# Optimization experiments

Hardware: AMD Instinct MI355X
Metric: run time of the kernel (lower is better)

Reference implementation:

```python
import jax, jax.numpy as jnp
import numpy as np

N_WIRES = 6
DIM = 1 << N_WIRES  # 64, equals input channel dim C for amplitude encoding
HID = N_WIRES       # hidden_dim = len(ops)


def _rx(theta):
    c = jnp.cos(theta / 2).astype(jnp.complex64)
    s = jnp.sin(theta / 2).astype(jnp.complex64)
    return jnp.stack([jnp.stack([c, -1j * s]), jnp.stack([-1j * s, c])])


def _ry(theta):
    c = jnp.cos(theta / 2).astype(jnp.complex64)
    s = jnp.sin(theta / 2).astype(jnp.complex64)
    return jnp.stack([jnp.stack([c, -s]), jnp.stack([s, c])])


def _apply_1q(state, U, wire):
    # state: (N, 2, 2, ..., 2); apply 2x2 U on qubit axis wire+1
    s = jnp.moveaxis(state, wire + 1, 1)
    s = jnp.einsum('ab,nb...->na...', U, s)
    return jnp.moveaxis(s, 1, wire + 1)


def _apply_cnot(state, c, t):
    # flip target axis where control bit == 1
    s = jnp.moveaxis(state, (c + 1, t + 1), (1, 2))
    s = jnp.concatenate([s[:, :1], jnp.flip(s[:, 1:2], axis=2)], axis=1)
    return jnp.moveaxis(s, (1, 2), (c + 1, t + 1))


def _expval_z(state, wire):
    # <Z_wire> = P(bit=0) - P(bit=1)
    p = state.real ** 2 + state.imag ** 2
    p = jnp.moveaxis(p, wire + 1, 1).reshape(p.shape[0], 2, -1)
    return p[:, 0].sum(-1) - p[:, 1].sum(-1)


def _value_layer(x_flat, params, qk):
    # amplitude encoding: normalize input into state amplitudes (C == DIM)
    norm = jnp.linalg.norm(x_flat, axis=-1, keepdims=True)
    psi = (x_flat / norm).astype(jnp.complex64)
    state = psi.reshape((x_flat.shape[0],) + (2,) * N_WIRES)
    rx0, ry0, ry1 = params[0], params[1], params[2]
    for j in range(N_WIRES):
        state = _apply_1q(state, _rx(rx0[j]), j)
        state = _apply_1q(state, _ry(ry0[j]), j)
    for j in range(N_WIRES):
        state = _apply_cnot(state, j, (j + 1) % N_WIRES)
    for j in range(N_WIRES):
        state = _apply_1q(state, _ry(ry1[j]), j)
    if qk:
        z0 = _expval_z(state, 0)
        return jnp.stack([z0] * HID, axis=-1)  # qk=True replicates wire-0 <Z>
    return jnp.stack([_expval_z(state, w) for w in range(N_WIRES)], axis=-1)


def setup_inputs() -> dict:
    key = jax.random.key(0)
    k1, k2, k3, k4 = jax.random.split(key, 4)
    B, T, C = 16, 2048, DIM
    return {
        'x': jax.random.normal(k1, (B, T, C), dtype=jnp.float32),
        'params_q': jax.random.normal(k2, (3, N_WIRES), dtype=jnp.float32),
        'params_k': jax.random.normal(k3, (3, N_WIRES), dtype=jnp.float32),
        'params_v': jax.random.normal(k4, (3, N_WIRES), dtype=jnp.float32),
    }


def reference(x, params_q, params_k, params_v):
    B, T, C = x.shape
    xf = x.reshape(B * T, C)
    q = _value_layer(xf, params_q, True).reshape(B, T, HID)
    k = _value_layer(xf, params_k, True).reshape(B, T, HID)
    v = _value_layer(xf, params_v, False).reshape(B, T, HID)
    scores = jnp.einsum('btd,bsd->bts', q, k) / jnp.sqrt(jnp.float32(HID))
    attn = jax.nn.softmax(scores, axis=-1)
    return jnp.einsum('bts,bsd->btd', attn, v)
```

## Files before the change

kernel.cpp:

```cpp
#include <hip/hip_runtime.h>
#include <math.h>

#define NWIRES 6
#define DIM 64
#define NTOK 32768
#define NBATCH 16
#define TPB 2048
#define NMOM 16
#define SQRT6F 2.4494897427831781f

__global__ void qsa_prep(const float* __restrict__ pq,
                         const float* __restrict__ pk,
                         const float* __restrict__ pv,
                         float* __restrict__ cs) {
    int i = threadIdx.x;
    if (i >= 54) return;
    int circ = i / 18, g = i % 18;
    const float* p = (circ == 0) ? pq : (circ == 1 ? pk : pv);
    float s, c;
    sincosf(0.5f * p[g], &s, &c);
    cs[i * 2 + 0] = c;
    cs[i * 2 + 1] = s;
}

__device__ __forceinline__ float pswap(float v) { return __shfl_xor(v, 1, 64); }

template<int M>
__device__ __forceinline__ void rx_l(float* re, float* im, float c, float s) {
#pragma unroll
    for (int i = 0; i < 32; ++i) {
        if (i & M) continue;
        int j = i | M;
        float r0 = re[i], i0 = im[i], r1 = re[j], i1 = im[j];
        re[i] = c * r0 + s * i1;
        im[i] = c * i0 - s * r1;
        re[j] = c * r1 + s * i0;
        im[j] = c * i1 - s * r0;
    }
}

template<int M>
__device__ __forceinline__ void ry_l(float* re, float* im, float c, float s) {
#pragma unroll
    for (int i = 0; i < 32; ++i) {
        if (i & M) continue;
        int j = i | M;
        float r0 = re[i], i0 = im[i], r1 = re[j], i1 = im[j];
        re[i] = c * r0 - s * r1;
        im[i] = c * i0 - s * i1;
        re[j] = c * r1 + s * r0;
        im[j] = c * i1 + s * i0;
    }
}

template<int MC, int MT>
__device__ __forceinline__ void cnot_l(float* re, float* im) {
#pragma unroll
    for (int i = 0; i < 32; ++i) {
        if (!(i & MC) || (i & MT)) continue;
        int j = i | MT;
        float tr = re[i]; re[i] = re[j]; re[j] = tr;
        float ti = im[i]; im[i] = im[j]; im[j] = ti;
    }
}

__device__ __forceinline__ void rx_s(float* re, float* im, float c, float s) {
#pragma unroll
    for (int i = 0; i < 32; ++i) {
        float pre = pswap(re[i]), pim = pswap(im[i]);
        re[i] = c * re[i] + s * pim;
        im[i] = c * im[i] - s * pre;
    }
}

__device__ __forceinline__ void ry_s(float* re, float* im, float c, float ss) {
#pragma unroll
    for (int i = 0; i < 32; ++i) {
        float pre = pswap(re[i]), pim = pswap(im[i]);
        re[i] = c * re[i] + ss * pre;
        im[i] = c * im[i] + ss * pim;
    }
}

__device__ __forceinline__ void cnot_c01(float* re, float* im, int p) {
#pragma unroll
    for (int i = 0; i < 32; ++i) {
        if (i & 16) continue;
        int j = i | 16;
        float r0 = re[i], r1 = re[j], i0 = im[i], i1 = im[j];
        re[i] = p ? r1 : r0;  re[j] = p ? r0 : r1;
        im[i] = p ? i1 : i0;  im[j] = p ? i0 : i1;
    }
}

__device__ __forceinline__ void cnot_c50(float* re, float* im) {
#pragma unroll
    for (int i = 1; i < 32; i += 2) {
        re[i] = pswap(re[i]);
        im[i] = pswap(im[i]);
    }
}

__global__ __attribute__((amdgpu_waves_per_eu(4, 8)))
__launch_bounds__(64) void qsa_sim(
        const float* __restrict__ x,
        const float* __restrict__ cs,
        float* __restrict__ zq,
        float* __restrict__ kv) {
    int g = blockIdx.x * 64 + threadIdx.x;
    int p = g & 1;
    int token = g >> 1;
    int circ = blockIdx.y;
    const float* P = cs + circ * 36;

    float re[32], im[32];
    const float4* xp4 = (const float4*)(x + (size_t)g * 32);
#pragma unroll
    for (int k = 0; k < 8; ++k) {
        float4 v = xp4[k];
        re[4*k+0] = v.x; re[4*k+1] = v.y; re[4*k+2] = v.z; re[4*k+3] = v.w;
        im[4*k+0] = 0.f; im[4*k+1] = 0.f; im[4*k+2] = 0.f; im[4*k+3] = 0.f;
    }
    float sgn = p ? 1.f : -1.f;

    rx_s(re, im, P[0], P[1]);
    rx_l<16>(re, im, P[2],  P[3]);
    rx_l< 8>(re, im, P[4],  P[5]);
    rx_l< 4>(re, im, P[6],  P[7]);
    rx_l< 2>(re, im, P[8],  P[9]);
    rx_l< 1>(re, im, P[10], P[11]);
    ry_s(re, im, P[12], sgn * P[13]);
    ry_l<16>(re, im, P[14], P[15]);
    ry_l< 8>(re, im, P[16], P[17]);
    ry_l< 4>(re, im, P[18], P[19]);
    ry_l< 2>(re, im, P[20], P[21]);
    ry_l< 1>(re, im, P[22], P[23]);
    cnot_c01(re, im, p);
    cnot_l<16, 8>(re, im);
    cnot_l< 8, 4>(re, im);
    cnot_l< 4, 2>(re, im);
    cnot_l< 2, 1>(re, im);
    cnot_c50(re, im);
    ry_s(re, im, P[24], sgn * P[25]);
    ry_l<16>(re, im, P[26], P[27]);
    ry_l< 8>(re, im, P[28], P[29]);
    ry_l< 4>(re, im, P[30], P[31]);
    ry_l< 2>(re, im, P[32], P[33]);
    ry_l< 1>(re, im, P[34], P[35]);

    float nl = 0.f, t1=0.f, t2=0.f, t3=0.f, t4=0.f, t5=0.f;
#pragma unroll
    for (int i = 0; i < 32; ++i) {
        float pi = re[i]*re[i] + im[i]*im[i];
        nl += pi;
        if (!(i & 16)) t1 += pi;
        if (!(i &  8)) t2 += pi;
        if (!(i &  4)) t3 += pi;
        if (!(i &  2)) t4 += pi;
        if (!(i &  1)) t5 += pi;
    }
    float np = pswap(nl);
    float norm2 = nl + np;
    float S0 = p ? np : nl;
    float inv = 1.0f / norm2;
    float z0 = (2.f * S0 - norm2) * inv;

    if (circ == 0) {
        if (p == 0) zq[token] = SQRT6F * z0;
    } else if (circ == 1) {
        if (p == 0) kv[(size_t)token * 8] = z0;
    } else {
        float S1 = t1 + pswap(t1);
        float S2 = t2 + pswap(t2);
        float S3 = t3 + pswap(t3);
        float S4 = t4 + pswap(t4);
        float S5 = t5 + pswap(t5);
        float z1 = (2.f*S1 - norm2) * inv;
        float z2 = (2.f*S2 - norm2) * inv;
        float z3 = (2.f*S3 - norm2) * inv;
        float z4 = (2.f*S4 - norm2) * inv;
        float z5 = (2.f*S5 - norm2) * inv;
        float* o = kv + (size_t)token * 8;
        if (p == 0) { o[1] = z0; o[2] = z1; o[3] = z2; }
        else        { o[4] = z3; o[5] = z4; o[6] = z5; }
    }
}

__global__ __attribute__((amdgpu_waves_per_eu(1, 2)))
__launch_bounds__(64) void qsa_moments_partial(
        const float* __restrict__ kv,
        float* __restrict__ mpart) {
    int blk = blockIdx.x;
    int b = blk >> 3, c = blk & 7;
    int lane = threadIdx.x;
    float S[NMOM], H[NMOM][6];
#pragma unroll
    for (int m = 0; m < NMOM; ++m) {
        S[m] = 0.f;
#pragma unroll
        for (int w = 0; w < 6; ++w) H[m][w] = 0.f;
    }
    const float* base = kv + ((size_t)(b * TPB + c * 256)) * 8;
#pragma unroll
    for (int r = 0; r < 4; ++r) {
        const float4* e = (const float4*)(base + (size_t)(r * 64 + lane) * 8);
        float4 e0 = e[0], e1 = e[1];
        float z = e0.x;
        float v0 = e0.y, v1 = e0.z, v2 = e0.w, v3 = e1.x, v4 = e1.y, v5 = e1.z;
        float pw = 1.f;
#pragma unroll
        for (int m = 0; m < NMOM; ++m) {
            S[m] += pw;
            H[m][0] += pw * v0; H[m][1] += pw * v1; H[m][2] += pw * v2;
            H[m][3] += pw * v3; H[m][4] += pw * v4; H[m][5] += pw * v5;
            pw *= z;
        }
    }
#pragma unroll
    for (int d = 32; d >= 1; d >>= 1) {
#pragma unroll
        for (int m = 0; m < NMOM; ++m) {
            S[m] += __shfl_xor(S[m], d, 64);
#pragma unroll
            for (int w = 0; w < 6; ++w) H[m][w] += __shfl_xor(H[m][w], d, 64);
        }
    }
    if (lane == 0) {
        float* o = mpart + (size_t)blk * 112;
#pragma unroll
        for (int m = 0; m < NMOM; ++m) {
            float* om = o + m * 7;
            om[0] = S[m];
            om[1] = H[m][0]; om[2] = H[m][1]; om[3] = H[m][2];
            om[4] = H[m][3]; om[5] = H[m][4]; om[6] = H[m][5];
        }
    }
}

__global__ void qsa_moments_combine(const float* __restrict__ mpart,
                                    float* __restrict__ mom) {
#pragma unroll
    for (int it = 0; it < 7; ++it) {
        int i = it * 256 + threadIdx.x;
        int b = i / 112, j = i % 112;
        float s = 0.f;
#pragma unroll
        for (int c = 0; c < 8; ++c) s += mpart[(size_t)(b * 8 + c) * 112 + j];
        mom[(size_t)b * 112 + j] = s;
    }
}

__global__ __launch_bounds__(256) void qsa_eval(
        const float* __restrict__ zq,
        const float* __restrict__ mom,
        float* __restrict__ out) {
    int t = blockIdx.x * 256 + threadIdx.x;
    int b = t >> 11;
    const float* M = mom + (size_t)b * 112;
    float a = zq[t];
    float den = 0.f, o0 = 0.f, o1 = 0.f, o2 = 0.f, o3 = 0.f, o4 = 0.f, o5 = 0.f;
    float pw = 1.f;
#pragma unroll
    for (int m = 0; m < NMOM; ++m) {
        const float* mm = M + m * 7;
        den += pw * mm[0];
        o0 += pw * mm[1]; o1 += pw * mm[2]; o2 += pw * mm[3];
        o3 += pw * mm[4]; o4 += pw * mm[5]; o5 += pw * mm[6];
        pw *= a * (1.0f / (m + 1));
    }
    float inv = 1.0f / den;
    float* o = out + (size_t)t * 6;
    float2* o2p = (float2*)o;
    o2p[0] = make_float2(o0 * inv, o1 * inv);
    o2p[1] = make_float2(o2 * inv, o3 * inv);
    o2p[2] = make_float2(o4 * inv, o5 * inv);
}

extern "C" void kernel_launch(void* const* d_in, const int* in_sizes, int n_in,
                              void* d_out, int out_size, void* d_ws, size_t ws_size,
                              hipStream_t stream) {
    const float* x  = (const float*)d_in[0];
    const float* pq = (const float*)d_in[1];
    const float* pk = (const float*)d_in[2];
    const float* pv = (const float*)d_in[3];
    float* w = (float*)d_ws;
    float* cs    = w;
    float* zq    = w + 128;
    float* kv    = w + 128 + NTOK;
    float* mpart = w + 128 + NTOK + NTOK * 8;
    float* mom   = mpart + 128 * 112;
    float* out   = (float*)d_out;

    qsa_prep<<<1, 64, 0, stream>>>(pq, pk, pv, cs);
    qsa_sim<<<dim3(NTOK * 2 / 64, 3), 64, 0, stream>>>(x, cs, zq, kv);
    qsa_moments_partial<<<NBATCH * 8, 64, 0, stream>>>(kv, mpart);
    qsa_moments_combine<<<1, 256, 0, stream>>>(mpart, mom);
    qsa_eval<<<NTOK / 256, 256, 0, stream>>>(zq, mom, out);
}
```

Baseline: 96.89 us.

## Split each token's state vector across four lanes instead of two

```diff
diff --git a/kernel.cpp b/kernel.cpp
--- a/kernel.cpp
+++ b/kernel.cpp
@@ -23,12 +23,13 @@
     cs[i * 2 + 1] = s;
 }
 
-__device__ __forceinline__ float pswap(float v) { return __shfl_xor(v, 1, 64); }
+template<int D>
+__device__ __forceinline__ float psw(float v) { return __shfl_xor(v, D, 64); }
 
 template<int M>
 __device__ __forceinline__ void rx_l(float* re, float* im, float c, float s) {
 #pragma unroll
-    for (int i = 0; i < 32; ++i) {
+    for (int i = 0; i < 16; ++i) {
         if (i & M) continue;
         int j = i | M;
         float r0 = re[i], i0 = im[i], r1 = re[j], i1 = im[j];
@@ -42,7 +43,7 @@
 template<int M>
 __device__ __forceinline__ void ry_l(float* re, float* im, float c, float s) {
 #pragma unroll
-    for (int i = 0; i < 32; ++i) {
+    for (int i = 0; i < 16; ++i) {
         if (i & M) continue;
         int j = i | M;
         float r0 = re[i], i0 = im[i], r1 = re[j], i1 = im[j];
@@ -56,7 +57,7 @@
 template<int MC, int MT>
 __device__ __forceinline__ void cnot_l(float* re, float* im) {
 #pragma unroll
-    for (int i = 0; i < 32; ++i) {
+    for (int i = 0; i < 16; ++i) {
         if (!(i & MC) || (i & MT)) continue;
         int j = i | MT;
         float tr = re[i]; re[i] = re[j]; re[j] = tr;
@@ -64,125 +65,120 @@
     }
 }
 
+template<int D>
 __device__ __forceinline__ void rx_s(float* re, float* im, float c, float s) {
 #pragma unroll
-    for (int i = 0; i < 32; ++i) {
-        float pre = pswap(re[i]), pim = pswap(im[i]);
+    for (int i = 0; i < 16; ++i) {
+        float pre = psw<D>(re[i]), pim = psw<D>(im[i]);
         re[i] = c * re[i] + s * pim;
         im[i] = c * im[i] - s * pre;
     }
 }
 
+template<int D>
 __device__ __forceinline__ void ry_s(float* re, float* im, float c, float ss) {
 #pragma unroll
-    for (int i = 0; i < 32; ++i) {
-        float pre = pswap(re[i]), pim = pswap(im[i]);
+    for (int i = 0; i < 16; ++i) {
+        float pre = psw<D>(re[i]), pim = psw<D>(im[i]);
         re[i] = c * re[i] + ss * pre;
         im[i] = c * im[i] + ss * pim;
     }
 }
 
-__device__ __forceinline__ void cnot_c01(float* re, float* im, int p) {
-#pragma unroll
-    for (int i = 0; i < 32; ++i) {
-        if (i & 16) continue;
-        int j = i | 16;
-        float r0 = re[i], r1 = re[j], i0 = im[i], i1 = im[j];
-        re[i] = p ? r1 : r0;  re[j] = p ? r0 : r1;
-        im[i] = p ? i1 : i0;  im[j] = p ? i0 : i1;
-    }
-}
-
-__device__ __forceinline__ void cnot_c50(float* re, float* im) {
-#pragma unroll
-    for (int i = 1; i < 32; i += 2) {
-        re[i] = pswap(re[i]);
-        im[i] = pswap(im[i]);
-    }
-}
-
-__global__ __attribute__((amdgpu_waves_per_eu(4, 8)))
-__launch_bounds__(64) void qsa_sim(
+__global__ __launch_bounds__(256) void qsa_sim(
         const float* __restrict__ x,
         const float* __restrict__ cs,
         float* __restrict__ zq,
         float* __restrict__ kv) {
-    int g = blockIdx.x * 64 + threadIdx.x;
-    int p = g & 1;
-    int token = g >> 1;
+    int g = blockIdx.x * 256 + threadIdx.x;
+    int l = g & 3;
+    int p0 = (l >> 1) & 1, p1 = l & 1;
+    int token = g >> 2;
     int circ = blockIdx.y;
     const float* P = cs + circ * 36;
 
-    float re[32], im[32];
-    const float4* xp4 = (const float4*)(x + (size_t)g * 32);
-#pragma unroll
-    for (int k = 0; k < 8; ++k) {
+    float re[16], im[16];
+    const float4* xp4 = (const float4*)(x + (size_t)g * 16);
+#pragma unroll
+    for (int k = 0; k < 4; ++k) {
         float4 v = xp4[k];
         re[4*k+0] = v.x; re[4*k+1] = v.y; re[4*k+2] = v.z; re[4*k+3] = v.w;
         im[4*k+0] = 0.f; im[4*k+1] = 0.f; im[4*k+2] = 0.f; im[4*k+3] = 0.f;
     }
-    float sgn = p ? 1.f : -1.f;
-
-    rx_s(re, im, P[0], P[1]);
-    rx_l<16>(re, im, P[2],  P[3]);
-    rx_l< 8>(re, im, P[4],  P[5]);
-    rx_l< 4>(re, im, P[6],  P[7]);
-    rx_l< 2>(re, im, P[8],  P[9]);
-    rx_l< 1>(re, im, P[10], P[11]);
-    ry_s(re, im, P[12], sgn * P[13]);
-    ry_l<16>(re, im, P[14], P[15]);
-    ry_l< 8>(re, im, P[16], P[17]);
-    ry_l< 4>(re, im, P[18], P[19]);
-    ry_l< 2>(re, im, P[20], P[21]);
-    ry_l< 1>(re, im, P[22], P[23]);
-    cnot_c01(re, im, p);
-    cnot_l<16, 8>(re, im);
-    cnot_l< 8, 4>(re, im);
-    cnot_l< 4, 2>(re, im);
-    cnot_l< 2, 1>(re, im);
-    cnot_c50(re, im);
-    ry_s(re, im, P[24], sgn * P[25]);
-    ry_l<16>(re, im, P[26], P[27]);
-    ry_l< 8>(re, im, P[28], P[29]);
-    ry_l< 4>(re, im, P[30], P[31]);
-    ry_l< 2>(re, im, P[32], P[33]);
-    ry_l< 1>(re, im, P[34], P[35]);
-
-    float nl = 0.f, t1=0.f, t2=0.f, t3=0.f, t4=0.f, t5=0.f;
-#pragma unroll
-    for (int i = 0; i < 32; ++i) {
+
+    rx_s<2>(re, im, P[0], P[1]);
+    rx_s<1>(re, im, P[2], P[3]);
+    rx_l<8>(re, im, P[4],  P[5]);
+    rx_l<4>(re, im, P[6],  P[7]);
+    rx_l<2>(re, im, P[8],  P[9]);
+    rx_l<1>(re, im, P[10], P[11]);
+    ry_s<2>(re, im, P[12], p0 ? P[13] : -P[13]);
+    ry_s<1>(re, im, P[14], p1 ? P[15] : -P[15]);
+    ry_l<8>(re, im, P[16], P[17]);
+    ry_l<4>(re, im, P[18], P[19]);
+    ry_l<2>(re, im, P[20], P[21]);
+    ry_l<1>(re, im, P[22], P[23]);
+
+#pragma unroll
+    for (int i = 0; i < 16; ++i) {
+        float tr = psw<1>(re[i]), ti = psw<1>(im[i]);
+        re[i] = p0 ? tr : re[i];
+        im[i] = p0 ? ti : im[i];
+    }
+#pragma unroll
+    for (int i = 0; i < 8; ++i) {
+        int j = i | 8;
+        float ra = re[i], rb = re[j], ia = im[i], ib = im[j];
+        re[i] = p1 ? rb : ra;  re[j] = p1 ? ra : rb;
+        im[i] = p1 ? ib : ia;  im[j] = p1 ? ia : ib;
+    }
+    cnot_l<8, 4>(re, im);
+    cnot_l<4, 2>(re, im);
+    cnot_l<2, 1>(re, im);
+#pragma unroll
+    for (int i = 1; i < 16; i += 2) {
+        re[i] = psw<2>(re[i]);
+        im[i] = psw<2>(im[i]);
+    }
+
+    ry_s<2>(re, im, P[24], p0 ? P[25] : -P[25]);
+    ry_s<1>(re, im, P[26], p1 ? P[27] : -P[27]);
+    ry_l<8>(re, im, P[28], P[29]);
+    ry_l<4>(re, im, P[30], P[31]);
+    ry_l<2>(re, im, P[32], P[33]);
+    ry_l<1>(re, im, P[34], P[35]);
+
+    float nl = 0.f, u2 = 0.f, u3 = 0.f, u4 = 0.f, u5 = 0.f;
+#pragma unroll
+    for (int i = 0; i < 16; ++i) {
         float pi = re[i]*re[i] + im[i]*im[i];
         nl += pi;
-        if (!(i & 16)) t1 += pi;
-        if (!(i &  8)) t2 += pi;
-        if (!(i &  4)) t3 += pi;
-        if (!(i &  2)) t4 += pi;
-        if (!(i &  1)) t5 += pi;
-    }
-    float np = pswap(nl);
-    float norm2 = nl + np;
-    float S0 = p ? np : nl;
+        if (!(i & 8)) u2 += pi;
+        if (!(i & 4)) u3 += pi;
+        if (!(i & 2)) u4 += pi;
+        if (!(i & 1)) u5 += pi;
+    }
+    auto qsum = [](float v) { v += psw<1>(v); v += psw<2>(v); return v; };
+    float norm2 = qsum(nl);
+    float S0 = qsum(p0 ? 0.f : nl);
     float inv = 1.0f / norm2;
     float z0 = (2.f * S0 - norm2) * inv;
 
     if (circ == 0) {
-        if (p == 0) zq[token] = SQRT6F * z0;
+        if (l == 0) zq[token] = SQRT6F * z0;
     } else if (circ == 1) {
-        if (p == 0) kv[(size_t)token * 8] = z0;
+        if (l == 0) kv[(size_t)token * 8] = z0;
     } else {
-        float S1 = t1 + pswap(t1);
-        float S2 = t2 + pswap(t2);
-        float S3 = t3 + pswap(t3);
-        float S4 = t4 + pswap(t4);
-        float S5 = t5 + pswap(t5);
+        float S1 = qsum(p1 ? 0.f : nl);
+        float S2 = qsum(u2), S3 = qsum(u3), S4 = qsum(u4), S5 = qsum(u5);
         float z1 = (2.f*S1 - norm2) * inv;
         float z2 = (2.f*S2 - norm2) * inv;
         float z3 = (2.f*S3 - norm2) * inv;
         float z4 = (2.f*S4 - norm2) * inv;
         float z5 = (2.f*S5 - norm2) * inv;
         float* o = kv + (size_t)token * 8;
-        if (p == 0) { o[1] = z0; o[2] = z1; o[3] = z2; }
-        else        { o[4] = z3; o[5] = z4; o[6] = z5; }
+        if (l == 0)      { o[1] = z0; o[2] = z1; o[3] = z2; }
+        else if (l == 1) { o[4] = z3; o[5] = z4; o[6] = z5; }
     }
 }
 
@@ -292,7 +288,7 @@
     float* out   = (float*)d_out;
 
     qsa_prep<<<1, 64, 0, stream>>>(pq, pk, pv, cs);
-    qsa_sim<<<dim3(NTOK * 2 / 64, 3), 64, 0, stream>>>(x, cs, zq, kv);
+    qsa_sim<<<dim3(NTOK * 4 / 256, 3), 256, 0, stream>>>(x, cs, zq, kv);
     qsa_moments_partial<<<NBATCH * 8, 64, 0, stream>>>(kv, mpart);
     qsa_moments_combine<<<1, 256, 0, stream>>>(mpart, mom);
     qsa_eval<<<NTOK / 256, 256, 0, stream>>>(zq, mom, out);
```

Result: no change. 95.14 us (-1.8%).
